# Kernel optimization log

Measured on AMD Instinct MI355X. Metric: run time of the kernel, lower is better.

Reference implementation:

```python
import jax, jax.numpy as jnp
import numpy as np

D_MODEL = 1024


def setup_inputs() -> dict:
    key = jax.random.key(0)
    ks = jax.random.split(key, 7)
    B, S, D = 4, 2048, D_MODEL
    scale = 1.0 / np.sqrt(D)
    inp = {
        "query": jax.random.normal(ks[0], (B, S, D), dtype=jnp.float32),
        "key": jax.random.normal(ks[1], (B, S, D), dtype=jnp.float32),
        "value": jax.random.normal(ks[2], (B, S, D), dtype=jnp.float32),
        # NOTE: original torch code applies query_projection to q, k AND v,
        # so only one projection weight (Wq) participates, plus output proj.
        "Wq": (jax.random.normal(ks[3], (D, D), dtype=jnp.float32) * scale),
        "bq": jnp.zeros((D,), dtype=jnp.float32),
        "Wo": (jax.random.normal(ks[4], (D, D), dtype=jnp.float32) * scale),
        "bo": jnp.zeros((D,), dtype=jnp.float32),
    }
    return inp


def reference(query, key, value, Wq, bq, Wo, bo):
    # Faithful to source: same projection (Wq, bq) used for q, k, v.
    q = jnp.einsum("bsd,de->bse", query, Wq) + bq   # (B, S, D)
    k = jnp.einsum("btd,de->bte", key, Wq) + bq     # (B, T, D)
    v = jnp.einsum("btd,de->bte", value, Wq) + bq   # (B, T, D)
    # No 1/sqrt(d) scaling in the original.
    score = jnp.einsum("bse,bte->bst", q, k)        # (B, S, T)
    weights = jax.nn.softmax(score, axis=-1)
    # Dropout is identity in eval / for a deterministic reference.
    ctx = jnp.einsum("bst,bte->bse", weights, v)    # (B, S, D)
    out = jnp.einsum("bse,ef->bsf", ctx, Wo) + bo   # (B, S, D)
    return (out, weights)
```

## Files before the change

kernel.cpp:

```cpp
#include <hip/hip_runtime.h>

typedef unsigned short u16;
typedef unsigned int u32;
typedef signed char i8;
typedef __bf16 bf16x8 __attribute__((ext_vector_type(8)));
typedef float f32x4 __attribute__((ext_vector_type(4)));
typedef int i32x4 __attribute__((ext_vector_type(4)));
typedef i8 i8x4 __attribute__((ext_vector_type(4)));
typedef u16 u16x8 __attribute__((ext_vector_type(8)));

#define AS1(p) ((const __attribute__((address_space(1))) void*)(p))
#define AS3(p) ((__attribute__((address_space(3))) void*)(p))

__device__ __forceinline__ u16 f2bf(float x) {
  u32 u = __float_as_uint(x);
  u32 r = u + 0x7fffu + ((u >> 16) & 1u);
  return (u16)(r >> 16);
}
__device__ __forceinline__ float bf2f(u16 h) {
  return __uint_as_float(((u32)h) << 16);
}

#define S_IN (8.0f / 127.0f)
#define S_W (0.25f / 127.0f)
#define S_QK (8.0f / 127.0f)
#define INV_S_IN (127.0f / 8.0f)
#define INV_S_W (508.0f)
#define INV_S_QK (127.0f / 8.0f)

__device__ __forceinline__ int2 q8i(float x, float inv_s) {
  float t = fminf(fmaxf(x * inv_s, -126.99f), 126.99f);
  float hf = rintf(t);
  float lf = fminf(fmaxf(rintf((t - hf) * 256.0f), -127.0f), 127.0f);
  return make_int2((int)hf, (int)lf);
}

__global__ __launch_bounds__(256) void prep_all(
    const float* __restrict__ q, const float* __restrict__ k,
    const float* __restrict__ value, const float* __restrict__ Wq,
    const float* __restrict__ Wo, i8* __restrict__ qh, i8* __restrict__ ql,
    i8* __restrict__ kh, i8* __restrict__ kl, u16* __restrict__ valT,
    i8* __restrict__ wqt_h, i8* __restrict__ wqt_l, u16* __restrict__ wot,
    u16* __restrict__ wq_b) {
  __shared__ float tileA[32][33];
  __shared__ float tileB[32][33];
  const int bid = blockIdx.x;
  const int tid = threadIdx.x;
  const int D = 1024;

  if (bid < 8192) {
    const int bx = bid & 31;
    const int by = (bid >> 5) & 63;
    const int bz = bid >> 11;
    const int tx = tid & 31, ty = tid >> 5;
    const int c0 = bx * 32, r0 = by * 32;
    const size_t zi = (size_t)bz * 2048 * 1024;
#pragma unroll
    for (int i = ty; i < 32; i += 8)
      tileA[i][tx] = value[zi + (size_t)(r0 + i) * D + (c0 + tx)];
    __syncthreads();
#pragma unroll
    for (int i = ty; i < 32; i += 8)
      valT[zi + (size_t)(c0 + i) * 2048 + (r0 + tx)] = f2bf(tileA[tx][i]);
  } else if (bid < 10240) {
    const int b2 = bid - 8192;
    const int n4 = 2097152;
    const int stride = 2048 * 256;
    for (int i = b2 * 256 + tid; i < n4; i += stride) {
      float4 x = ((const float4*)q)[i];
      float xs[4] = {x.x, x.y, x.z, x.w};
      i8x4 h, l;
#pragma unroll
      for (int e = 0; e < 4; ++e) {
        int2 r = q8i(xs[e], INV_S_IN);
        h[e] = (i8)r.x;
        l[e] = (i8)r.y;
      }
      ((i8x4*)qh)[i] = h;
      ((i8x4*)ql)[i] = l;
      x = ((const float4*)k)[i];
      float ys[4] = {x.x, x.y, x.z, x.w};
#pragma unroll
      for (int e = 0; e < 4; ++e) {
        int2 r = q8i(ys[e], INV_S_IN);
        h[e] = (i8)r.x;
        l[e] = (i8)r.y;
      }
      ((i8x4*)kh)[i] = h;
      ((i8x4*)kl)[i] = l;
    }
  } else {
    const int r = bid - 10240;
    const int bx = r & 31, by = r >> 5;
    const int tx = tid & 31, ty = tid >> 5;
    const int c0 = bx * 32, r0 = by * 32;
#pragma unroll
    for (int i = ty; i < 32; i += 8) {
      float xq = Wq[(size_t)(r0 + i) * D + c0 + tx];
      tileA[i][tx] = xq;
      wq_b[(size_t)(r0 + i) * D + c0 + tx] = f2bf(xq);
      tileB[i][tx] = Wo[(size_t)(r0 + i) * D + c0 + tx];
    }
    __syncthreads();
#pragma unroll
    for (int i = ty; i < 32; i += 8) {
      float x = tileA[tx][i];
      int2 rr = q8i(x, INV_S_W);
      size_t o = (size_t)(c0 + i) * D + r0 + tx;
      wqt_h[o] = (i8)rr.x;
      wqt_l[o] = (i8)rr.y;
      wot[o] = f2bf(tileB[tx][i]);
    }
  }
}

__global__ __launch_bounds__(256) void bqo_kernel(const float* __restrict__ bq,
                                                  const u16* __restrict__ wot,
                                                  const float* __restrict__ bo,
                                                  float* __restrict__ bqo,
                                                  int D) {
  const int f = blockIdx.x * 4 + (threadIdx.x >> 6);
  const int lane = threadIdx.x & 63;
  const u16* wr_ = wot + (size_t)f * D;
  float s = 0.f;
  for (int e = lane; e < D; e += 64) s += bq[e] * bf2f(wr_[e]);
#pragma unroll
  for (int off = 32; off; off >>= 1) s += __shfl_xor(s, off);
  if (lane == 0) bqo[f] = s + bo[f];
}

template <int EPI>
__global__ __launch_bounds__(256, 2) void gemm_bt(
    const u16* __restrict__ Ah, const u16* __restrict__ Bh,
    const float* __restrict__ bias, float* __restrict__ Cf,
    u16* __restrict__ Ch, int M, int N, int K,
    long long sA, long long sB, long long sC) {
  __shared__ alignas(16) u16 As[128 * 32];
  __shared__ alignas(16) u16 Bs[128 * 32];

  const int t = threadIdx.x;
  const int lane = t & 63;
  const int w = t >> 6;
  const int wr = w >> 1, wc = w & 1;

  const long long zb = blockIdx.z;
  const u16* pA = Ah + zb * sA;
  const u16* pB = Bh + zb * sB;

  const int m0 = blockIdx.x * 128;
  const int n0 = blockIdx.y * 128;

  f32x4 acc[4][4] = {};

  const int row0 = t >> 2;
  const int colS = (t & 3) * 8;
  const int lds0 = (t & ~63) * 8;
  const int lds1 = (256 + (t & ~63)) * 8;

  const size_t aoff0 = (size_t)(m0 + row0) * K + colS;
  const size_t aoff1 = (size_t)(m0 + row0 + 64) * K + colS;
  const size_t boff0 = (size_t)(n0 + row0) * K + colS;
  const size_t boff1 = (size_t)(n0 + row0 + 64) * K + colS;

  for (int k0 = 0; k0 < K; k0 += 32) {
    __syncthreads();
    __builtin_amdgcn_global_load_lds(AS1(pA + aoff0 + k0), AS3(&As[lds0]), 16, 0, 0);
    __builtin_amdgcn_global_load_lds(AS1(pA + aoff1 + k0), AS3(&As[lds1]), 16, 0, 0);
    __builtin_amdgcn_global_load_lds(AS1(pB + boff0 + k0), AS3(&Bs[lds0]), 16, 0, 0);
    __builtin_amdgcn_global_load_lds(AS1(pB + boff1 + k0), AS3(&Bs[lds1]), 16, 0, 0);
    __syncthreads();

    const int fr = lane & 15;
    const int kc = (lane >> 4) * 8;
    bf16x8 a[4], b[4];
#pragma unroll
    for (int i = 0; i < 4; ++i)
      a[i] = *(const bf16x8*)&As[(wr * 64 + i * 16 + fr) * 32 + kc];
#pragma unroll
    for (int j = 0; j < 4; ++j)
      b[j] = *(const bf16x8*)&Bs[(wc * 64 + j * 16 + fr) * 32 + kc];
#pragma unroll
    for (int i = 0; i < 4; ++i)
#pragma unroll
      for (int j = 0; j < 4; ++j)
        acc[i][j] = __builtin_amdgcn_mfma_f32_16x16x32_bf16(a[i], b[j], acc[i][j], 0, 0, 0);
  }

  const int er = (lane >> 4) * 4;
  const int ec = lane & 15;
#pragma unroll
  for (int j = 0; j < 4; ++j) {
    const int gcol = n0 + wc * 64 + j * 16 + ec;
    const float bv = bias ? bias[gcol] : 0.0f;
#pragma unroll
    for (int i = 0; i < 4; ++i) {
      const int grow0 = m0 + wr * 64 + i * 16 + er;
#pragma unroll
      for (int r = 0; r < 4; ++r) {
        const float x = acc[i][j][r] + bv;
        const size_t off = (size_t)zb * sC + (size_t)(grow0 + r) * N + gcol;
        if constexpr (EPI == 0) Cf[off] = x;
        else Ch[off] = f2bf(x);
      }
    }
  }
}

#define STG_I(DSTBASE, SH, SL, ROWBASE, KREAL)                                 \
  do {                                                                         \
    const i8* s0_ = (sc < 4 ? (SH) : (SL)) +                                   \
                    (size_t)((ROWBASE) + sr) * K + (KREAL) + ((sc & 3) << 4);  \
    const i8* s1_ = s0_ + (size_t)64 * K;                                      \
    __builtin_amdgcn_global_load_lds(AS1(s0_), AS3(&lds8[(DSTBASE) + ldsB]), 16, 0, 0); \
    __builtin_amdgcn_global_load_lds(AS1(s1_), AS3(&lds8[(DSTBASE) + 8192 + ldsB]), 16, 0, 0); \
  } while (0)

#define LDA_IV(BUF, QM, AH, AL)                                                \
  do {                                                                         \
    const int base_ = (BUF) * 49152;                                           \
    _Pragma("unroll") for (int i_ = 0; i_ < 4; ++i_) {                         \
      const int r_ = (QM) * 128 + wr * 64 + i_ * 16 + fr;                      \
      AH[i_] = *(const i32x4*)&lds8[base_ + r_ * 128 + ((ksl ^ (r_ & 7)) << 4)]; \
      AL[i_] = *(const i32x4*)&lds8[base_ + r_ * 128 + (((4 + ksl) ^ (r_ & 7)) << 4)]; \
    }                                                                          \
  } while (0)

#define LDB_IV(BUF)                                                            \
  do {                                                                         \
    const int base_ = (BUF) * 49152 + 32768;                                   \
    _Pragma("unroll") for (int j_ = 0; j_ < 2; ++j_) {                         \
      const int r_ = wc * 32 + (j_) * 16 + fr;                                 \
      bh[j_] = *(const i32x4*)&lds8[base_ + r_ * 128 + ((ksl ^ (r_ & 7)) << 4)]; \
      bl[j_] = *(const i32x4*)&lds8[base_ + r_ * 128 + (((4 + ksl) ^ (r_ & 7)) << 4)]; \
    }                                                                          \
  } while (0)

#define MMA_IV(QM, AH, AL)                                                     \
  do {                                                                         \
    _Pragma("unroll") for (int j_ = 0; j_ < 2; ++j_) {                         \
      _Pragma("unroll") for (int i_ = 0; i_ < 4; ++i_) {                       \
        accH[(QM) * 4 + i_][j_] = __builtin_amdgcn_mfma_i32_16x16x64_i8(       \
            AH[i_], bh[j_], accH[(QM) * 4 + i_][j_], 0, 0, 0);                 \
        accX[(QM) * 4 + i_][j_] = __builtin_amdgcn_mfma_i32_16x16x64_i8(       \
            AH[i_], bl[j_], accX[(QM) * 4 + i_][j_], 0, 0, 0);                 \
        accX[(QM) * 4 + i_][j_] = __builtin_amdgcn_mfma_i32_16x16x64_i8(       \
            AL[i_], bh[j_], accX[(QM) * 4 + i_][j_], 0, 0, 0);                 \
      }                                                                        \
    }                                                                          \
  } while (0)

template <int EPI>
__global__ __launch_bounds__(512, 2) void gemm8i(
    const i8* __restrict__ Ah, const i8* __restrict__ Al,
    const i8* __restrict__ Bh, const i8* __restrict__ Bl,
    const float* __restrict__ bias, float sAB, float* __restrict__ Cf,
    i8* __restrict__ Ch, i8* __restrict__ Cl, int M, int N, int K,
    long long sA, long long sB, long long sC) {
  extern __shared__ i8 lds8[];

  const int tt = threadIdx.x;
  const int lane = tt & 63;
  const int wv = tt >> 6;
  const int wr = wv >> 2;
  const int wc = wv & 3;
  const int fr = lane & 15;
  const int ksl = lane >> 4;

  const long long zb = blockIdx.z;
  const i8* pAh = Ah + zb * sA;
  const i8* pAl = Al + zb * sA;
  const i8* pBh = Bh + zb * sB;
  const i8* pBl = Bl + zb * sB;
  const int m0 = blockIdx.x * 256;
  const int n0 = blockIdx.y * 128;

  const int sr = tt >> 3;
  const int ss = tt & 7;
  const int sc = ss ^ (sr & 7);
  const int ldsB = (tt & ~63) * 16;

  i32x4 accH[8][2] = {};
  i32x4 accX[8][2] = {};
  i32x4 ah0[4], al0[4], ah1[4], al1[4], bh[2], bl[2];

  const int NT = K / 64;
  const int NITER = NT / 2;

  STG_I(0, pAh, pAl, m0, 0);
  STG_I(16384, pAh, pAl, m0 + 128, 0);
  STG_I(32768, pBh, pBl, n0, 0);
  STG_I(49152, pAh, pAl, m0, 64);
  STG_I(49152 + 16384, pAh, pAl, m0 + 128, 64);
  STG_I(49152 + 32768, pBh, pBl, n0, 64);
  asm volatile("s_waitcnt vmcnt(6)" ::: "memory");
  __builtin_amdgcn_s_barrier();

  for (int it = 0; it < NITER; ++it) {
    const int t0 = 2 * it;
    const int k2 = (t0 + 2 < NT ? t0 + 2 : NT - 1) * 64;
    const int k3 = (t0 + 3 < NT ? t0 + 3 : NT - 1) * 64;

    LDA_IV(0, 0, ah0, al0);
    LDB_IV(0);
    LDA_IV(0, 1, ah1, al1);
    MMA_IV(0, ah0, al0);
    MMA_IV(1, ah1, al1);
    asm volatile("s_waitcnt lgkmcnt(0)" ::: "memory");
    __builtin_amdgcn_s_barrier();
    STG_I(0, pAh, pAl, m0, k2);
    STG_I(16384, pAh, pAl, m0 + 128, k2);
    STG_I(32768, pBh, pBl, n0, k2);
    asm volatile("s_waitcnt vmcnt(6)" ::: "memory");
    __builtin_amdgcn_s_barrier();

    LDA_IV(1, 0, ah0, al0);
    LDB_IV(1);
    LDA_IV(1, 1, ah1, al1);
    MMA_IV(0, ah0, al0);
    MMA_IV(1, ah1, al1);
    asm volatile("s_waitcnt lgkmcnt(0)" ::: "memory");
    __builtin_amdgcn_s_barrier();
    STG_I(49152, pAh, pAl, m0, k3);
    STG_I(49152 + 16384, pAh, pAl, m0 + 128, k3);
    STG_I(49152 + 32768, pBh, pBl, n0, k3);
    asm volatile("s_waitcnt vmcnt(6)" ::: "memory");
    __builtin_amdgcn_s_barrier();
  }

  const int er = (lane >> 4) * 4;
  const int ec = lane & 15;
#pragma unroll
  for (int fi = 0; fi < 8; ++fi) {
    const int grow0 = m0 + (fi >> 2) * 128 + wr * 64 + (fi & 3) * 16 + er;
#pragma unroll
    for (int j = 0; j < 2; ++j) {
      const int gcol = n0 + wc * 32 + j * 16 + ec;
      const float bv = bias ? bias[gcol] : 0.0f;
#pragma unroll
      for (int r = 0; r < 4; ++r) {
        const float x =
            sAB * ((float)accH[fi][j][r] + (float)accX[fi][j][r] * 0.00390625f) + bv;
        const size_t off = (size_t)zb * sC + (size_t)(grow0 + r) * N + gcol;
        if constexpr (EPI == 0) {
          Cf[off] = x;
        } else {
          int2 qq = q8i(x, INV_S_QK);
          Ch[off] = (i8)qq.x;
          Cl[off] = (i8)qq.y;
        }
      }
    }
  }
}

#define STG_P(DSTBASE, SRC, ROWBASE, KREAL)                                    \
  do {                                                                         \
    const u16* s0_ = (SRC) + (size_t)((ROWBASE) + sr) * K + (KREAL) + (sc << 3); \
    const u16* s1_ = s0_ + (size_t)64 * K;                                     \
    __builtin_amdgcn_global_load_lds(AS1(s0_), AS3(&lds[(DSTBASE) + ldsW]), 16, 0, 0); \
    __builtin_amdgcn_global_load_lds(AS1(s1_), AS3(&lds[(DSTBASE) + 4096 + ldsW]), 16, 0, 0); \
  } while (0)

#define LDA_P(BUF, QM, S, DST)                                                 \
  do {                                                                         \
    const int base_ = (BUF) * 24576 + (QM) * 8192;                             \
    _Pragma("unroll") for (int i_ = 0; i_ < 4; ++i_) {                         \
      const int r_ = wr * 64 + i_ * 16 + fr;                                   \
      DST[i_] = *(const bf16x8*)&lds[base_ + r_ * 64 + (((((S) * 4 + ksl)) ^ (r_ & 7)) << 3)]; \
    }                                                                          \
  } while (0)

#define LDB_P(BUF, S, DST)                                                     \
  do {                                                                         \
    const int base_ = (BUF) * 24576 + 16384;                                   \
    _Pragma("unroll") for (int j_ = 0; j_ < 2; ++j_) {                         \
      const int r_ = wc * 32 + j_ * 16 + fr;                                   \
      DST[j_] = *(const bf16x8*)&lds[base_ + r_ * 64 + (((((S) * 4 + ksl)) ^ (r_ & 7)) << 3)]; \
    }                                                                          \
  } while (0)

#define MMA_P(QM, A_, B_)                                                      \
  do {                                                                         \
    _Pragma("unroll") for (int i_ = 0; i_ < 4; ++i_) {                         \
      _Pragma("unroll") for (int j_ = 0; j_ < 2; ++j_) {                       \
        acc[(QM) * 4 + i_][j_] = __builtin_amdgcn_mfma_f32_16x16x32_bf16(      \
            A_[i_], B_[j_], acc[(QM) * 4 + i_][j_], 0, 0, 0);                  \
      }                                                                        \
    }                                                                          \
  } while (0)

template <int EPI>
__global__ __launch_bounds__(512, 2) void gemm8p(
    const u16* __restrict__ A, const u16* __restrict__ B,
    const float* __restrict__ bias, float* __restrict__ Cf,
    u16* __restrict__ Ch, int M, int N, int K,
    long long sA, long long sB, long long sC) {
  extern __shared__ u16 lds[];

  const int tt = threadIdx.x;
  const int lane = tt & 63;
  const int wv = tt >> 6;
  const int wr = wv >> 2;
  const int wc = wv & 3;
  const int fr = lane & 15;
  const int ksl = lane >> 4;

  const long long zb = blockIdx.z;
  const u16* pA = A + zb * sA;
  const u16* pB = B + zb * sB;
  const int m0 = blockIdx.x * 256;
  const int n0 = blockIdx.y * 128;

  const int sr = tt >> 3;
  const int ss = tt & 7;
  const int sc = ss ^ (sr & 7);
  const int ldsW = (tt & ~63) * 8;

  f32x4 acc[8][2] = {};
  bf16x8 a0[4], a1[4], a2[4], a3[4], b0[2], b1[2];

  const int NT = K / 64;

  STG_P(16384, pB, n0, 0);
  STG_P(0, pA, m0, 0);
  STG_P(8192, pA, m0 + 128, 0);
  STG_P(24576 + 16384, pB, n0, 64);
  STG_P(24576 + 0, pA, m0, 64);
  STG_P(24576 + 8192, pA, m0 + 128, 64);
  asm volatile("s_waitcnt vmcnt(6)" ::: "memory");
  __builtin_amdgcn_s_barrier();

  for (int it = 0; it < NT; ++it) {
    const int cur = it & 1;
    const int nb = cur * 24576;
    const int kf = (it + 2 < NT ? it + 2 : NT - 1) * 64;

    LDA_P(cur, 0, 0, a0);
    LDA_P(cur, 0, 1, a1);
    LDB_P(cur, 0, b0);
    LDB_P(cur, 1, b1);
    LDA_P(cur, 1, 0, a2);
    LDA_P(cur, 1, 1, a3);
    MMA_P(0, a0, b0);
    MMA_P(0, a1, b1);
    MMA_P(1, a2, b0);
    MMA_P(1, a3, b1);
    asm volatile("s_waitcnt lgkmcnt(0)" ::: "memory");
    __builtin_amdgcn_s_barrier();
    STG_P(nb + 16384, pB, n0, kf);
    STG_P(nb + 0, pA, m0, kf);
    STG_P(nb + 8192, pA, m0 + 128, kf);
    asm volatile("s_waitcnt vmcnt(6)" ::: "memory");
    __builtin_amdgcn_s_barrier();
  }

  const int er = (lane >> 4) * 4;
  const int ec = lane & 15;
#pragma unroll
  for (int fi = 0; fi < 8; ++fi) {
    const int qm = fi >> 2, i = fi & 3;
    const int grow0 = m0 + qm * 128 + wr * 64 + i * 16 + er;
#pragma unroll
    for (int j = 0; j < 2; ++j) {
      const int gcol = n0 + wc * 32 + j * 16 + ec;
      const float bv = bias ? bias[gcol] : 0.0f;
#pragma unroll
      for (int r = 0; r < 4; ++r) {
        const float x = acc[fi][j][r] + bv;
        const size_t off = (size_t)zb * sC + (size_t)(grow0 + r) * N + gcol;
        if constexpr (EPI == 0) Cf[off] = x;
        else Ch[off] = f2bf(x);
      }
    }
  }
}

__global__ __launch_bounds__(256) void softmax_rows_v(float* __restrict__ S,
                                                      u16* __restrict__ P) {
  const int T = 2048;
  const size_t row = blockIdx.x;
  float* sr = S + row * T;
  u16* prow = P + row * T;
  const int t = threadIdx.x;
  const int w = t >> 6, lane = t & 63;
  __shared__ float red[8];

  float4 r0 = ((const float4*)(sr + t * 8))[0];
  float4 r1 = ((const float4*)(sr + t * 8))[1];
  float v[8] = {r0.x, r0.y, r0.z, r0.w, r1.x, r1.y, r1.z, r1.w};
  float mx = -1e30f;
#pragma unroll
  for (int i = 0; i < 8; ++i) mx = fmaxf(mx, v[i]);
#pragma unroll
  for (int off = 32; off; off >>= 1) mx = fmaxf(mx, __shfl_xor(mx, off));
  if (lane == 0) red[w] = mx;
  __syncthreads();
  mx = fmaxf(fmaxf(red[0], red[1]), fmaxf(red[2], red[3]));

  float s = 0.f;
#pragma unroll
  for (int i = 0; i < 8; ++i) {
    v[i] = __expf(v[i] - mx);
    s += v[i];
  }
#pragma unroll
  for (int off = 32; off; off >>= 1) s += __shfl_xor(s, off);
  if (lane == 0) red[4 + w] = s;
  __syncthreads();
  s = (red[4] + red[5]) + (red[6] + red[7]);
  const float inv = 1.0f / s;

  u16x8 pv;
#pragma unroll
  for (int i = 0; i < 8; ++i) {
    v[i] *= inv;
    pv[i] = f2bf(v[i]);
  }
  float4* wr4 = (float4*)(sr + t * 8);
  wr4[0] = make_float4(v[0], v[1], v[2], v[3]);
  wr4[1] = make_float4(v[4], v[5], v[6], v[7]);
  ((u16x8*)prow)[t] = pv;
}

extern "C" void kernel_launch(void* const* d_in, const int* in_sizes, int n_in,
                              void* d_out, int out_size, void* d_ws,
                              size_t ws_size, hipStream_t stream) {
  (void)in_sizes; (void)n_in; (void)out_size; (void)ws_size;
  const float* query = (const float*)d_in[0];
  const float* key   = (const float*)d_in[1];
  const float* value = (const float*)d_in[2];
  const float* Wq    = (const float*)d_in[3];
  const float* bq    = (const float*)d_in[4];
  const float* Wo    = (const float*)d_in[5];
  const float* bo    = (const float*)d_in[6];

  const int S = 2048, D = 1024;
  const size_t n = (size_t)4 * S * D;

  float* out = (float*)d_out;
  float* wts = out + n;

  char* ws = (char*)d_ws;
  i8* wqt_h = (i8*)(ws);
  i8* wqt_l = (i8*)(ws + (1ull << 20));
  u16* wot  = (u16*)(ws + (2ull << 20));
  u16* wq_b = (u16*)(ws + (4ull << 20));
  u16* wqoT = (u16*)(ws + (6ull << 20));
  float* bqo = (float*)(ws + (8ull << 20));
  i8* QKh = (i8*)(ws + (9ull << 20));
  i8* QKl = (i8*)(ws + (25ull << 20));
  u16* tmp = (u16*)(ws + (41ull << 20));
  u16* P = (u16*)(ws + (9ull << 20));

  i8* ah = (i8*)wts;
  i8* al = ah + 2 * n;
  u16* valT = (u16*)out;

  hipFuncSetAttribute((const void*)&gemm8i<2>,
                      hipFuncAttributeMaxDynamicSharedMemorySize, 98304);
  hipFuncSetAttribute((const void*)&gemm8i<0>,
                      hipFuncAttributeMaxDynamicSharedMemorySize, 98304);
  hipFuncSetAttribute((const void*)&gemm8p<1>,
                      hipFuncAttributeMaxDynamicSharedMemorySize, 98304);
  hipFuncSetAttribute((const void*)&gemm8p<0>,
                      hipFuncAttributeMaxDynamicSharedMemorySize, 98304);

  prep_all<<<11264, 256, 0, stream>>>(query, key, value, Wq, Wo, ah, al,
                                      ah + n, al + n, valT, wqt_h, wqt_l, wot,
                                      wq_b);
  gemm_bt<1><<<dim3(8, 8, 1), 256, 0, stream>>>(
      wot, wq_b, nullptr, nullptr, wqoT, 1024, 1024, 1024, 0, 0, 0);
  bqo_kernel<<<256, 256, 0, stream>>>(bq, wot, bo, bqo, D);
  gemm8i<2><<<dim3(64, 8, 1), 512, 98304, stream>>>(
      ah, al, wqt_h, wqt_l, bq, S_IN * S_W, nullptr, QKh, QKl,
      16384, 1024, 1024, 0, 0, 0);
  gemm8i<0><<<dim3(8, 16, 4), 512, 98304, stream>>>(
      QKh, QKl, QKh + n, QKl + n, nullptr, S_QK * S_QK, wts, nullptr, nullptr,
      2048, 2048, 1024, (long long)S * D, (long long)S * D, (long long)S * S);
  softmax_rows_v<<<8192, 256, 0, stream>>>(wts, P);
  gemm8p<1><<<dim3(8, 8, 4), 512, 98304, stream>>>(
      P, valT, nullptr, nullptr, tmp, 2048, 1024, 2048, (long long)S * S,
      (long long)D * S, (long long)S * D);
  gemm8p<0><<<dim3(32, 8, 1), 512, 98304, stream>>>(
      tmp, wqoT, bqo, out, nullptr, 8192, 1024, 1024, 0, 0, 0);
}
```

Before: 275.0 us.

## Remap GEMM warps to a 4x2 grid of 64x64 tiles

Both the int8-split GEMM and the bf16 GEMM change their wave layout from 2x4 waves covering 128x32 each to 4x2 waves covering 64x64 each over the 256x128 block tile. Each wave now reads fewer A rows and more B rows from LDS, so per-MFMA LDS fragment traffic drops and operands are reused more evenly, and register use for fragments changes. Accumulator count per wave stays the same, but the mapping of LDS reads, the bank pattern and the epilogue store pattern all change.

```diff
diff --git a/kernel.cpp b/kernel.cpp
--- a/kernel.cpp
+++ b/kernel.cpp
@@ -215,36 +215,36 @@
     __builtin_amdgcn_global_load_lds(AS1(s1_), AS3(&lds8[(DSTBASE) + 8192 + ldsB]), 16, 0, 0); \
   } while (0)
 
-#define LDA_IV(BUF, QM, AH, AL)                                                \
+#define LDA_IV(BUF)                                                            \
   do {                                                                         \
     const int base_ = (BUF) * 49152;                                           \
     _Pragma("unroll") for (int i_ = 0; i_ < 4; ++i_) {                         \
-      const int r_ = (QM) * 128 + wr * 64 + i_ * 16 + fr;                      \
-      AH[i_] = *(const i32x4*)&lds8[base_ + r_ * 128 + ((ksl ^ (r_ & 7)) << 4)]; \
-      AL[i_] = *(const i32x4*)&lds8[base_ + r_ * 128 + (((4 + ksl) ^ (r_ & 7)) << 4)]; \
+      const int r_ = wr * 64 + i_ * 16 + fr;                                   \
+      ah[i_] = *(const i32x4*)&lds8[base_ + r_ * 128 + ((ksl ^ (r_ & 7)) << 4)]; \
+      al[i_] = *(const i32x4*)&lds8[base_ + r_ * 128 + (((4 + ksl) ^ (r_ & 7)) << 4)]; \
     }                                                                          \
   } while (0)
 
 #define LDB_IV(BUF)                                                            \
   do {                                                                         \
     const int base_ = (BUF) * 49152 + 32768;                                   \
-    _Pragma("unroll") for (int j_ = 0; j_ < 2; ++j_) {                         \
-      const int r_ = wc * 32 + (j_) * 16 + fr;                                 \
+    _Pragma("unroll") for (int j_ = 0; j_ < 4; ++j_) {                         \
+      const int r_ = wc * 64 + j_ * 16 + fr;                                   \
       bh[j_] = *(const i32x4*)&lds8[base_ + r_ * 128 + ((ksl ^ (r_ & 7)) << 4)]; \
       bl[j_] = *(const i32x4*)&lds8[base_ + r_ * 128 + (((4 + ksl) ^ (r_ & 7)) << 4)]; \
     }                                                                          \
   } while (0)
 
-#define MMA_IV(QM, AH, AL)                                                     \
-  do {                                                                         \
-    _Pragma("unroll") for (int j_ = 0; j_ < 2; ++j_) {                         \
+#define MMA_IV()                                                               \
+  do {                                                                         \
+    _Pragma("unroll") for (int j_ = 0; j_ < 4; ++j_) {                         \
       _Pragma("unroll") for (int i_ = 0; i_ < 4; ++i_) {                       \
-        accH[(QM) * 4 + i_][j_] = __builtin_amdgcn_mfma_i32_16x16x64_i8(       \
-            AH[i_], bh[j_], accH[(QM) * 4 + i_][j_], 0, 0, 0);                 \
-        accX[(QM) * 4 + i_][j_] = __builtin_amdgcn_mfma_i32_16x16x64_i8(       \
-            AH[i_], bl[j_], accX[(QM) * 4 + i_][j_], 0, 0, 0);                 \
-        accX[(QM) * 4 + i_][j_] = __builtin_amdgcn_mfma_i32_16x16x64_i8(       \
-            AL[i_], bh[j_], accX[(QM) * 4 + i_][j_], 0, 0, 0);                 \
+        accH[i_][j_] = __builtin_amdgcn_mfma_i32_16x16x64_i8(                  \
+            ah[i_], bh[j_], accH[i_][j_], 0, 0, 0);                            \
+        accX[i_][j_] = __builtin_amdgcn_mfma_i32_16x16x64_i8(                  \
+            ah[i_], bl[j_], accX[i_][j_], 0, 0, 0);                            \
+        accX[i_][j_] = __builtin_amdgcn_mfma_i32_16x16x64_i8(                  \
+            al[i_], bh[j_], accX[i_][j_], 0, 0, 0);                            \
       }                                                                        \
     }                                                                          \
   } while (0)
@@ -261,8 +261,8 @@
   const int tt = threadIdx.x;
   const int lane = tt & 63;
   const int wv = tt >> 6;
-  const int wr = wv >> 2;
-  const int wc = wv & 3;
+  const int wr = wv >> 1;
+  const int wc = wv & 1;
   const int fr = lane & 15;
   const int ksl = lane >> 4;
 
@@ -279,9 +279,9 @@
   const int sc = ss ^ (sr & 7);
   const int ldsB = (tt & ~63) * 16;
 
-  i32x4 accH[8][2] = {};
-  i32x4 accX[8][2] = {};
-  i32x4 ah0[4], al0[4], ah1[4], al1[4], bh[2], bl[2];
+  i32x4 accH[4][4] = {};
+  i32x4 accX[4][4] = {};
+  i32x4 ah[4], al[4], bh[4], bl[4];
 
   const int NT = K / 64;
   const int NITER = NT / 2;
@@ -300,11 +300,9 @@
     const int k2 = (t0 + 2 < NT ? t0 + 2 : NT - 1) * 64;
     const int k3 = (t0 + 3 < NT ? t0 + 3 : NT - 1) * 64;
 
-    LDA_IV(0, 0, ah0, al0);
+    LDA_IV(0);
     LDB_IV(0);
-    LDA_IV(0, 1, ah1, al1);
-    MMA_IV(0, ah0, al0);
-    MMA_IV(1, ah1, al1);
+    MMA_IV();
     asm volatile("s_waitcnt lgkmcnt(0)" ::: "memory");
     __builtin_amdgcn_s_barrier();
     STG_I(0, pAh, pAl, m0, k2);
@@ -313,11 +311,9 @@
     asm volatile("s_waitcnt vmcnt(6)" ::: "memory");
     __builtin_amdgcn_s_barrier();
 
-    LDA_IV(1, 0, ah0, al0);
+    LDA_IV(1);
     LDB_IV(1);
-    LDA_IV(1, 1, ah1, al1);
-    MMA_IV(0, ah0, al0);
-    MMA_IV(1, ah1, al1);
+    MMA_IV();
     asm volatile("s_waitcnt lgkmcnt(0)" ::: "memory");
     __builtin_amdgcn_s_barrier();
     STG_I(49152, pAh, pAl, m0, k3);
@@ -330,16 +326,16 @@
   const int er = (lane >> 4) * 4;
   const int ec = lane & 15;
 #pragma unroll
-  for (int fi = 0; fi < 8; ++fi) {
-    const int grow0 = m0 + (fi >> 2) * 128 + wr * 64 + (fi & 3) * 16 + er;
-#pragma unroll
-    for (int j = 0; j < 2; ++j) {
-      const int gcol = n0 + wc * 32 + j * 16 + ec;
+  for (int i = 0; i < 4; ++i) {
+    const int grow0 = m0 + wr * 64 + i * 16 + er;
+#pragma unroll
+    for (int j = 0; j < 4; ++j) {
+      const int gcol = n0 + wc * 64 + j * 16 + ec;
       const float bv = bias ? bias[gcol] : 0.0f;
 #pragma unroll
       for (int r = 0; r < 4; ++r) {
         const float x =
-            sAB * ((float)accH[fi][j][r] + (float)accX[fi][j][r] * 0.00390625f) + bv;
+            sAB * ((float)accH[i][j][r] + (float)accX[i][j][r] * 0.00390625f) + bv;
         const size_t off = (size_t)zb * sC + (size_t)(grow0 + r) * N + gcol;
         if constexpr (EPI == 0) {
           Cf[off] = x;
@@ -361,9 +357,9 @@
     __builtin_amdgcn_global_load_lds(AS1(s1_), AS3(&lds[(DSTBASE) + 4096 + ldsW]), 16, 0, 0); \
   } while (0)
 
-#define LDA_P(BUF, QM, S, DST)                                                 \
-  do {                                                                         \
-    const int base_ = (BUF) * 24576 + (QM) * 8192;                             \
+#define LDA_P(BUF, S, DST)                                                     \
+  do {                                                                         \
+    const int base_ = (BUF) * 24576;                                           \
     _Pragma("unroll") for (int i_ = 0; i_ < 4; ++i_) {                         \
       const int r_ = wr * 64 + i_ * 16 + fr;                                   \
       DST[i_] = *(const bf16x8*)&lds[base_ + r_ * 64 + (((((S) * 4 + ksl)) ^ (r_ & 7)) << 3)]; \
@@ -373,18 +369,18 @@
 #define LDB_P(BUF, S, DST)                                                     \
   do {                                                                         \
     const int base_ = (BUF) * 24576 + 16384;                                   \
-    _Pragma("unroll") for (int j_ = 0; j_ < 2; ++j_) {                         \
-      const int r_ = wc * 32 + j_ * 16 + fr;                                   \
+    _Pragma("unroll") for (int j_ = 0; j_ < 4; ++j_) {                         \
+      const int r_ = wc * 64 + j_ * 16 + fr;                                   \
       DST[j_] = *(const bf16x8*)&lds[base_ + r_ * 64 + (((((S) * 4 + ksl)) ^ (r_ & 7)) << 3)]; \
     }                                                                          \
   } while (0)
 
-#define MMA_P(QM, A_, B_)                                                      \
+#define MMA_P(A_, B_)                                                          \
   do {                                                                         \
     _Pragma("unroll") for (int i_ = 0; i_ < 4; ++i_) {                         \
-      _Pragma("unroll") for (int j_ = 0; j_ < 2; ++j_) {                       \
-        acc[(QM) * 4 + i_][j_] = __builtin_amdgcn_mfma_f32_16x16x32_bf16(      \
-            A_[i_], B_[j_], acc[(QM) * 4 + i_][j_], 0, 0, 0);                  \
+      _Pragma("unroll") for (int j_ = 0; j_ < 4; ++j_) {                       \
+        acc[i_][j_] = __builtin_amdgcn_mfma_f32_16x16x32_bf16(                 \
+            A_[i_], B_[j_], acc[i_][j_], 0, 0, 0);                             \
       }                                                                        \
     }                                                                          \
   } while (0)
@@ -400,8 +396,8 @@
   const int tt = threadIdx.x;
   const int lane = tt & 63;
   const int wv = tt >> 6;
-  const int wr = wv >> 2;
-  const int wc = wv & 3;
+  const int wr = wv >> 1;
+  const int wc = wv & 1;
   const int fr = lane & 15;
   const int ksl = lane >> 4;
 
@@ -416,8 +412,8 @@
   const int sc = ss ^ (sr & 7);
   const int ldsW = (tt & ~63) * 8;
 
-  f32x4 acc[8][2] = {};
-  bf16x8 a0[4], a1[4], a2[4], a3[4], b0[2], b1[2];
+  f32x4 acc[4][4] = {};
+  bf16x8 a0[4], a1[4], b0[4], b1[4];
 
   const int NT = K / 64;
 
@@ -435,16 +431,12 @@
     const int nb = cur * 24576;
     const int kf = (it + 2 < NT ? it + 2 : NT - 1) * 64;
 
-    LDA_P(cur, 0, 0, a0);
-    LDA_P(cur, 0, 1, a1);
+    LDA_P(cur, 0, a0);
     LDB_P(cur, 0, b0);
+    LDA_P(cur, 1, a1);
     LDB_P(cur, 1, b1);
-    LDA_P(cur, 1, 0, a2);
-    LDA_P(cur, 1, 1, a3);
-    MMA_P(0, a0, b0);
-    MMA_P(0, a1, b1);
-    MMA_P(1, a2, b0);
-    MMA_P(1, a3, b1);
+    MMA_P(a0, b0);
+    MMA_P(a1, b1);
     asm volatile("s_waitcnt lgkmcnt(0)" ::: "memory");
     __builtin_amdgcn_s_barrier();
     STG_P(nb + 16384, pB, n0, kf);
@@ -457,16 +449,15 @@
   const int er = (lane >> 4) * 4;
   const int ec = lane & 15;
 #pragma unroll
-  for (int fi = 0; fi < 8; ++fi) {
-    const int qm = fi >> 2, i = fi & 3;
-    const int grow0 = m0 + qm * 128 + wr * 64 + i * 16 + er;
-#pragma unroll
-    for (int j = 0; j < 2; ++j) {
-      const int gcol = n0 + wc * 32 + j * 16 + ec;
+  for (int i = 0; i < 4; ++i) {
+    const int grow0 = m0 + wr * 64 + i * 16 + er;
+#pragma unroll
+    for (int j = 0; j < 4; ++j) {
+      const int gcol = n0 + wc * 64 + j * 16 + ec;
       const float bv = bias ? bias[gcol] : 0.0f;
 #pragma unroll
       for (int r = 0; r < 4; ++r) {
-        const float x = acc[fi][j][r] + bv;
+        const float x = acc[i][j][r] + bv;
         const size_t off = (size_t)zb * sC + (size_t)(grow0 + r) * N + gcol;
         if constexpr (EPI == 0) Cf[off] = x;
         else Ch[off] = f2bf(x);
```

Result: no change. 272.4 us (-0.9%).
